# Performance work log

Hardware: AMD Instinct MI355X
Metric: run time of the kernel (lower is better)

Reference implementation:

```python
import jax, jax.numpy as jnp
import numpy as np

N_NODES = 50000
N_EDGES = 600000
CHANNELS = 128
HEADS = 8


def setup_inputs() -> dict:
    key = jax.random.key(0)
    k1, k2, k3 = jax.random.split(key, 3)
    x = jax.random.normal(k1, (N_NODES, CHANNELS), dtype=jnp.float32)
    edge_index = jax.random.randint(k2, (2, N_EDGES), 0, N_NODES, dtype=jnp.int32)
    att = jax.random.normal(k3, (HEADS, 2 * (CHANNELS // HEADS)), dtype=jnp.float32)
    return {"x": x, "edge_index": edge_index, "att": att}


def reference(x, edge_index, att):
    # x: [N, C], edge_index: [2, E], att: [H, 2*D] with D = C // H
    src, dst = edge_index[0], edge_index[1]
    n = x.shape[0]
    h = att.shape[0]
    d = att.shape[1] // 2

    x_src = x[src].reshape(-1, h, d)   # [E, H, D]
    x_dst = x[dst].reshape(-1, h, d)   # [E, H, D]

    # (cat([x_src, x_dst]) * att).sum(-1) == x_src @ att[:, :D] + x_dst @ att[:, D:]
    a_src, a_dst = att[:, :d], att[:, d:]
    alpha = jnp.einsum('ehd,hd->eh', x_src, a_src) + jnp.einsum('ehd,hd->eh', x_dst, a_dst)
    alpha = jnp.where(alpha >= 0, alpha, 0.2 * alpha)  # LeakyReLU(0.2)

    # segment softmax over dst; torch scatter_reduce amax includes the zero init,
    # so the per-node max is max(segment_max, 0)
    seg_max = jax.ops.segment_max(alpha, dst, num_segments=n)  # [N, H]
    seg_max = jnp.maximum(seg_max, 0.0)
    alpha = jnp.exp(alpha - seg_max[dst])
    seg_sum = jax.ops.segment_sum(alpha, dst, num_segments=n)  # [N, H]
    alpha = alpha / jnp.maximum(seg_sum[dst], 1e-10)

    # weighted scatter-add of source features
    weighted = x_src * alpha[..., None]                        # [E, H, D]
    out = jax.ops.segment_sum(weighted, dst, num_segments=n)   # [N, H, D]
    return out.reshape(n, -1)
```

## Files before the change

### kernel.cpp

```cpp
#include <hip/hip_runtime.h>

#define N_NODES  50000
#define N_EDGES  600000
#define CHANNELS 128
#define HEADS    8
#define HEAD_DIM 16
#define CAP      64

#define NBINS    256
#define CHUNK_E  1024
#define NCHUNK   ((N_EDGES + CHUNK_E - 1) / CHUNK_E)
#define SEGCAP   2816
#define NPB      200
#define BPAD     16

#define LOGIT_VB ((N_NODES * (CHANNELS / 8)) / 256)
#define WPB      4

__device__ __forceinline__ unsigned bf16rne(float f) {
    unsigned u = __float_as_uint(f);
    return (u + 0x7FFFu + ((u >> 16) & 1u)) >> 16;
}

__global__ void logit_kernel(const float* __restrict__ x,
                             const float* __restrict__ att,
                             float*          __restrict__ ls8,
                             float*          __restrict__ ld8,
                             unsigned short* __restrict__ xb,
                             int*            __restrict__ bincnt_p) {
    if (blockIdx.x == LOGIT_VB) {
        bincnt_p[threadIdx.x * BPAD] = 0;
        return;
    }
    int gid = blockIdx.x * 256 + threadIdx.x;
    int n  = gid >> 4;
    int c8 = gid & 15;
    int h  = c8 >> 1;
    int j8 = c8 & 1;

    const float4* xp = (const float4*)x + (size_t)gid * 2;
    float4 v0 = xp[0], v1 = xp[1];

    uint4 pk;
    pk.x = bf16rne(v0.x) | (bf16rne(v0.y) << 16);
    pk.y = bf16rne(v0.z) | (bf16rne(v0.w) << 16);
    pk.z = bf16rne(v1.x) | (bf16rne(v1.y) << 16);
    pk.w = bf16rne(v1.z) | (bf16rne(v1.w) << 16);
    ((uint4*)xb)[gid] = pk;

    const float4* att4 = (const float4*)att;
    float4 as0 = att4[h * 8 + j8 * 2],     as1 = att4[h * 8 + j8 * 2 + 1];
    float4 ad0 = att4[h * 8 + 4 + j8 * 2], ad1 = att4[h * 8 + 5 + j8 * 2];
    float ts = v0.x*as0.x + v0.y*as0.y + v0.z*as0.z + v0.w*as0.w
             + v1.x*as1.x + v1.y*as1.y + v1.z*as1.z + v1.w*as1.w;
    float td = v0.x*ad0.x + v0.y*ad0.y + v0.z*ad0.z + v0.w*ad0.w
             + v1.x*ad1.x + v1.y*ad1.y + v1.z*ad1.z + v1.w*ad1.w;
    ts += __shfl_xor(ts, 1, 2);
    td += __shfl_xor(td, 1, 2);
    if (j8 == 0) {
        ls8[n * HEADS + h] = ts;
        ld8[n * HEADS + h] = td;
    }
}

__global__ void binscatter_kernel(const int* __restrict__ src,
                                  const int* __restrict__ dst,
                                  int*       __restrict__ bincnt_p,
                                  unsigned*  __restrict__ ebuf) {
    __shared__ int lh[NBINS];
    __shared__ int lbase[NBINS];
    int b = blockIdx.x;
    int t = threadIdx.x;
    lh[t] = 0;
    __syncthreads();
    int base = b * CHUNK_E;
    unsigned rec[4], bn[4];
#pragma unroll
    for (int k = 0; k < 4; ++k) {
        int e = base + t + k * 256;
        if (e < N_EDGES) {
            int d = dst[e];
            int s = src[e];
            unsigned bin = (unsigned)(d * NBINS) / N_NODES;
            bn[k]  = bin;
            rec[k] = (unsigned)s | ((unsigned)d << 16);
            atomicAdd(&lh[bin], 1);
        } else bn[k] = 0xFFFFFFFFu;
    }
    __syncthreads();
    int cnt_bin = lh[t];
    __syncthreads();
    lbase[t] = (cnt_bin > 0) ? atomicAdd(&bincnt_p[t * BPAD], cnt_bin) : 0;
    lh[t] = 0;
    __syncthreads();
#pragma unroll
    for (int k = 0; k < 4; ++k) {
        if (bn[k] != 0xFFFFFFFFu) {
            int r = atomicAdd(&lh[bn[k]], 1) + lbase[bn[k]];
            if (r < SEGCAP)
                ebuf[(size_t)bn[k] * SEGCAP + r] = rec[k];
        }
    }
}

__global__ void bucket_kernel(const unsigned* __restrict__ ebuf,
                              const int*      __restrict__ bincnt_p,
                              int*            __restrict__ cursor,
                              unsigned short* __restrict__ bucket) {
    __shared__ unsigned short rows[NPB * CAP];
    __shared__ int lcnt[NPB];
    int b = blockIdx.x;
    int t = threadIdx.x;
    int n0 = (b * N_NODES + NBINS - 1) / NBINS;
    int n1 = ((b + 1) * N_NODES + NBINS - 1) / NBINS;
    int nn = n1 - n0;
    if (t < NPB) lcnt[t] = 0;
    __syncthreads();
    int cnt = min(bincnt_p[b * BPAD], SEGCAP);
    for (int i = t; i < cnt; i += 256) {
        unsigned rec = ebuf[(size_t)b * SEGCAP + i];
        int s = (int)(rec & 0xFFFFu);
        int d = (int)(rec >> 16);
        int pos = atomicAdd(&lcnt[d - n0], 1);
        if (pos < CAP) rows[(d - n0) * CAP + pos] = (unsigned short)s;
    }
    __syncthreads();
    int nq = nn * (CAP * 2 / 16);
    uint4* gdst = (uint4*)(bucket + (size_t)n0 * CAP);
    const uint4* lsrc = (const uint4*)rows;
    for (int i = t; i < nq; i += 256) gdst[i] = lsrc[i];
    if (t < nn) cursor[n0 + t] = lcnt[t];
}

__global__ void fused_gat_kernel(const unsigned short* __restrict__ xb,
                                 const float* __restrict__ ls8,
                                 const float* __restrict__ ld8,
                                 const int*   __restrict__ cursor,
                                 const unsigned short* __restrict__ bucket,
                                 float*       __restrict__ out) {
    __shared__ float s_p[WPB * CAP * HEADS];

    int wave = threadIdx.x >> 6;
    int lane = threadIdx.x & 63;
    int n = blockIdx.x * WPB + wave;
    if (n >= N_NODES) return;
    int h = lane >> 3;
    int j = lane & 7;
    int r   = lane >> 4;
    int l16 = lane & 15;
    int h2  = l16 >> 1;

    int   cnt_raw = cursor[n];
    int   myidx   = (int)bucket[(size_t)n * CAP + lane];
    float ldst    = ld8[n * HEADS + h];
    int cnt = (cnt_raw > CAP) ? CAP : cnt_raw;

    float* sp = s_p + wave * (CAP * HEADS);

    float av[8];
    float mymax = -1e30f;
#pragma unroll
    for (int k = 0; k < 8; ++k) {
        int i = j + 8 * k;
        av[k] = -1e30f;
        if (i < cnt) {
            int   s  = __shfl(myidx, i);
            float lg = ls8[s * HEADS + h] + ldst;
            float a  = (lg >= 0.0f) ? lg : 0.2f * lg;
            av[k] = a;
            mymax = fmaxf(mymax, a);
        }
    }
#pragma unroll
    for (int o = 4; o >= 1; o >>= 1) mymax = fmaxf(mymax, __shfl_xor(mymax, o, 8));
    float m = fmaxf(mymax, 0.0f);

    float myl = 0.0f;
#pragma unroll
    for (int k = 0; k < 8; ++k) {
        int i = j + 8 * k;
        if (i < cnt) {
            float p = __expf(av[k] - m);
            sp[i * HEADS + h] = p;
            myl += p;
        }
    }
#pragma unroll
    for (int o = 4; o >= 1; o >>= 1) myl += __shfl_xor(myl, o, 8);

#define LO16(u) __uint_as_float((u) << 16)
#define HI16(u) __uint_as_float((u) & 0xFFFF0000u)
#define LP(kq) ( ((const uint4*)(xb + (size_t)__shfl(myidx, ((4*(kq)+r) < cnt) ? (4*(kq)+r) : 0) * CHANNELS))[l16] )
    uint4 q[4];
#pragma unroll
    for (int k = 0; k < 4; ++k) q[k] = LP(k);

    float a0 = 0.f, a1 = 0.f, a2 = 0.f, a3 = 0.f;
    float a4 = 0.f, a5 = 0.f, a6 = 0.f, a7 = 0.f;
    int nquad = (cnt + 3) >> 2;
    int k = 0;
    for (; k + 2 <= nquad; k += 2) {
#pragma unroll
        for (int u = 0; u < 2; ++u) {
            int e4 = 4 * (k + u) + r;
            float p = (e4 < cnt) ? sp[e4 * HEADS + h2] : 0.0f;
            uint4 qq = q[u];
            a0 += p * LO16(qq.x);
            a1 += p * HI16(qq.x);
            a2 += p * LO16(qq.y);
            a3 += p * HI16(qq.y);
            a4 += p * LO16(qq.z);
            a5 += p * HI16(qq.z);
            a6 += p * LO16(qq.w);
            a7 += p * HI16(qq.w);
        }
        q[0] = q[2]; q[1] = q[3];
        q[2] = LP(k + 4);
        q[3] = LP(k + 5);
    }
    for (; k < nquad; ++k) {
        int e4 = 4 * k + r;
        float p = (e4 < cnt) ? sp[e4 * HEADS + h2] : 0.0f;
        uint4 qq = q[0];
        a0 += p * LO16(qq.x);
        a1 += p * HI16(qq.x);
        a2 += p * LO16(qq.y);
        a3 += p * HI16(qq.y);
        a4 += p * LO16(qq.z);
        a5 += p * HI16(qq.z);
        a6 += p * LO16(qq.w);
        a7 += p * HI16(qq.w);
        q[0] = q[1]; q[1] = q[2]; q[2] = q[3];
    }
#undef LP
#undef LO16
#undef HI16

    a0 += __shfl_xor(a0, 16); a0 += __shfl_xor(a0, 32);
    a1 += __shfl_xor(a1, 16); a1 += __shfl_xor(a1, 32);
    a2 += __shfl_xor(a2, 16); a2 += __shfl_xor(a2, 32);
    a3 += __shfl_xor(a3, 16); a3 += __shfl_xor(a3, 32);
    a4 += __shfl_xor(a4, 16); a4 += __shfl_xor(a4, 32);
    a5 += __shfl_xor(a5, 16); a5 += __shfl_xor(a5, 32);
    a6 += __shfl_xor(a6, 16); a6 += __shfl_xor(a6, 32);
    a7 += __shfl_xor(a7, 16); a7 += __shfl_xor(a7, 32);

    float denom = __shfl(myl, h2 * 8);
    float inv = 1.0f / fmaxf(denom, 1e-10f);

    if (lane < 16) {
        float4 o0 = make_float4(a0 * inv, a1 * inv, a2 * inv, a3 * inv);
        float4 o1 = make_float4(a4 * inv, a5 * inv, a6 * inv, a7 * inv);
        float4* op = (float4*)(out + (size_t)n * CHANNELS) + l16 * 2;
        op[0] = o0;
        op[1] = o1;
    }
}

extern "C" void kernel_launch(void* const* d_in, const int* in_sizes, int n_in,
                              void* d_out, int out_size, void* d_ws, size_t ws_size,
                              hipStream_t stream) {
    const float* x   = (const float*)d_in[0];
    const int*   ei  = (const int*)  d_in[1];
    const float* att = (const float*)d_in[2];
    const int* src = ei;
    const int* dst = ei + N_EDGES;
    float* out = (float*)d_out;

    int*            bincnt_p = (int*)d_ws;
    unsigned*       ebuf     = (unsigned*)(bincnt_p + (size_t)NBINS * BPAD);
    int*            cursor   = (int*)(ebuf + (size_t)NBINS * SEGCAP);
    unsigned short* bucket   = (unsigned short*)(cursor + N_NODES);
    float*          ls8      = (float*)(bucket + (size_t)N_NODES * CAP);
    float*          ld8      = ls8 + (size_t)N_NODES * HEADS;
    unsigned short* xb       = (unsigned short*)(ld8 + (size_t)N_NODES * HEADS);

    logit_kernel<<<LOGIT_VB + 1, 256, 0, stream>>>(x, att, ls8, ld8, xb, bincnt_p);
    binscatter_kernel<<<NCHUNK, 256, 0, stream>>>(src, dst, bincnt_p, ebuf);
    bucket_kernel<<<NBINS, 256, 0, stream>>>(ebuf, bincnt_p, cursor, bucket);
    fused_gat_kernel<<<(N_NODES + WPB - 1) / WPB, 64 * WPB, 0, stream>>>(
        xb, ls8, ld8, cursor, bucket, out);
}
```

Baseline: 143.0 us.

## Fuse binning with logit prep and bucketing with aggregation into two kernels

The pipeline drops from four kernels to two. Edge binning now runs in the same launch as the logit/bf16 conversion, writing into fixed per-(bin,chunk) slots with per-chunk counts, which removes the global atomics and the zeroing step. The bucket build is fused into the aggregation kernel, so each block builds its node rows in shared memory and consumes them directly instead of writing and re-reading a global bucket array. In exchange, only 1024 blocks of 4 waves do the aggregation, each looping over about 49 nodes, which may lower parallelism and load balance. Per-chunk slot caps (24) could also silently drop edges when a chunk is skewed.

Result: faster. 136.4 us (-4.6%).

```diff
diff --git a/kernel.cpp b/kernel.cpp
--- a/kernel.cpp
+++ b/kernel.cpp
@@ -7,32 +7,59 @@
 #define HEAD_DIM 16
 #define CAP      64
 
-#define NBINS    256
-#define CHUNK_E  1024
+#define NBINS    1024
+#define CHUNK_E  4096
 #define NCHUNK   ((N_EDGES + CHUNK_E - 1) / CHUNK_E)
-#define SEGCAP   2816
-#define NPB      200
-#define BPAD     16
+#define CAPC     24
+#define NPB      52
 
 #define LOGIT_VB ((N_NODES * (CHANNELS / 8)) / 256)
-#define WPB      4
+#define NW       4
 
 __device__ __forceinline__ unsigned bf16rne(float f) {
     unsigned u = __float_as_uint(f);
     return (u + 0x7FFFu + ((u >> 16) & 1u)) >> 16;
 }
 
-__global__ void logit_kernel(const float* __restrict__ x,
-                             const float* __restrict__ att,
-                             float*          __restrict__ ls8,
-                             float*          __restrict__ ld8,
-                             unsigned short* __restrict__ xb,
-                             int*            __restrict__ bincnt_p) {
-    if (blockIdx.x == LOGIT_VB) {
-        bincnt_p[threadIdx.x * BPAD] = 0;
+__global__ void prep_kernel(const float* __restrict__ x,
+                            const float* __restrict__ att,
+                            const int*   __restrict__ src,
+                            const int*   __restrict__ dst,
+                            float*          __restrict__ ls8,
+                            float*          __restrict__ ld8,
+                            unsigned short* __restrict__ xb,
+                            unsigned*       __restrict__ ebuf,
+                            int*            __restrict__ cc) {
+    int b = blockIdx.x;
+    int t = threadIdx.x;
+    if (b < NCHUNK) {
+        __shared__ int lh[NBINS];
+#pragma unroll
+        for (int k = 0; k < NBINS / 256; ++k) lh[t + k * 256] = 0;
+        __syncthreads();
+        int base = b * CHUNK_E;
+#pragma unroll 4
+        for (int k = 0; k < CHUNK_E / 256; ++k) {
+            int e = base + t + k * 256;
+            if (e < N_EDGES) {
+                int d = dst[e];
+                int s = src[e];
+                unsigned bin = ((unsigned)d * NBINS) / N_NODES;
+                int r = atomicAdd(&lh[bin], 1);
+                if (r < CAPC)
+                    ebuf[((size_t)bin * NCHUNK + b) * CAPC + r] =
+                        (unsigned)s | ((unsigned)d << 16);
+            }
+        }
+        __syncthreads();
+#pragma unroll
+        for (int k = 0; k < NBINS / 256; ++k) {
+            int bin = t + k * 256;
+            cc[(size_t)bin * NCHUNK + b] = min(lh[bin], CAPC);
+        }
         return;
     }
-    int gid = blockIdx.x * 256 + threadIdx.x;
+    int gid = (b - NCHUNK) * 256 + t;
     int n  = gid >> 4;
     int c8 = gid & 15;
     int h  = c8 >> 1;
@@ -63,148 +90,121 @@
     }
 }
 
-__global__ void binscatter_kernel(const int* __restrict__ src,
-                                  const int* __restrict__ dst,
-                                  int*       __restrict__ bincnt_p,
-                                  unsigned*  __restrict__ ebuf) {
-    __shared__ int lh[NBINS];
-    __shared__ int lbase[NBINS];
-    int b = blockIdx.x;
-    int t = threadIdx.x;
-    lh[t] = 0;
-    __syncthreads();
-    int base = b * CHUNK_E;
-    unsigned rec[4], bn[4];
-#pragma unroll
-    for (int k = 0; k < 4; ++k) {
-        int e = base + t + k * 256;
-        if (e < N_EDGES) {
-            int d = dst[e];
-            int s = src[e];
-            unsigned bin = (unsigned)(d * NBINS) / N_NODES;
-            bn[k]  = bin;
-            rec[k] = (unsigned)s | ((unsigned)d << 16);
-            atomicAdd(&lh[bin], 1);
-        } else bn[k] = 0xFFFFFFFFu;
-    }
-    __syncthreads();
-    int cnt_bin = lh[t];
-    __syncthreads();
-    lbase[t] = (cnt_bin > 0) ? atomicAdd(&bincnt_p[t * BPAD], cnt_bin) : 0;
-    lh[t] = 0;
-    __syncthreads();
-#pragma unroll
-    for (int k = 0; k < 4; ++k) {
-        if (bn[k] != 0xFFFFFFFFu) {
-            int r = atomicAdd(&lh[bn[k]], 1) + lbase[bn[k]];
-            if (r < SEGCAP)
-                ebuf[(size_t)bn[k] * SEGCAP + r] = rec[k];
-        }
-    }
-}
-
-__global__ void bucket_kernel(const unsigned* __restrict__ ebuf,
-                              const int*      __restrict__ bincnt_p,
-                              int*            __restrict__ cursor,
-                              unsigned short* __restrict__ bucket) {
+__global__ void aggregate_kernel(const unsigned* __restrict__ ebuf,
+                                 const int*      __restrict__ cc,
+                                 const unsigned short* __restrict__ xb,
+                                 const float* __restrict__ ls8,
+                                 const float* __restrict__ ld8,
+                                 float*       __restrict__ out) {
     __shared__ unsigned short rows[NPB * CAP];
-    __shared__ int lcnt[NPB];
+    __shared__ int   lcnt[NPB];
+    __shared__ int   lcc[NCHUNK];
+    __shared__ float s_p[NW * CAP * HEADS];
+
     int b = blockIdx.x;
     int t = threadIdx.x;
     int n0 = (b * N_NODES + NBINS - 1) / NBINS;
     int n1 = ((b + 1) * N_NODES + NBINS - 1) / NBINS;
     int nn = n1 - n0;
     if (t < NPB) lcnt[t] = 0;
+    if (t < NCHUNK) lcc[t] = cc[(size_t)b * NCHUNK + t];
     __syncthreads();
-    int cnt = min(bincnt_p[b * BPAD], SEGCAP);
-    for (int i = t; i < cnt; i += 256) {
-        unsigned rec = ebuf[(size_t)b * SEGCAP + i];
-        int s = (int)(rec & 0xFFFFu);
-        int d = (int)(rec >> 16);
-        int pos = atomicAdd(&lcnt[d - n0], 1);
-        if (pos < CAP) rows[(d - n0) * CAP + pos] = (unsigned short)s;
+
+    const unsigned* seg = ebuf + (size_t)b * NCHUNK * CAPC;
+    for (int p = t; p < NCHUNK * CAPC; p += 256) {
+        int c    = p / CAPC;
+        int slot = p - c * CAPC;
+        if (slot < lcc[c]) {
+            unsigned rec = seg[p];
+            int s = (int)(rec & 0xFFFFu);
+            int d = (int)(rec >> 16);
+            int pos = atomicAdd(&lcnt[d - n0], 1);
+            if (pos < CAP) rows[(d - n0) * CAP + pos] = (unsigned short)s;
+        }
     }
     __syncthreads();
-    int nq = nn * (CAP * 2 / 16);
-    uint4* gdst = (uint4*)(bucket + (size_t)n0 * CAP);
-    const uint4* lsrc = (const uint4*)rows;
-    for (int i = t; i < nq; i += 256) gdst[i] = lsrc[i];
-    if (t < nn) cursor[n0 + t] = lcnt[t];
-}
-
-__global__ void fused_gat_kernel(const unsigned short* __restrict__ xb,
-                                 const float* __restrict__ ls8,
-                                 const float* __restrict__ ld8,
-                                 const int*   __restrict__ cursor,
-                                 const unsigned short* __restrict__ bucket,
-                                 float*       __restrict__ out) {
-    __shared__ float s_p[WPB * CAP * HEADS];
-
-    int wave = threadIdx.x >> 6;
-    int lane = threadIdx.x & 63;
-    int n = blockIdx.x * WPB + wave;
-    if (n >= N_NODES) return;
+
+    int wave = t >> 6;
+    int lane = t & 63;
     int h = lane >> 3;
     int j = lane & 7;
     int r   = lane >> 4;
     int l16 = lane & 15;
     int h2  = l16 >> 1;
-
-    int   cnt_raw = cursor[n];
-    int   myidx   = (int)bucket[(size_t)n * CAP + lane];
-    float ldst    = ld8[n * HEADS + h];
-    int cnt = (cnt_raw > CAP) ? CAP : cnt_raw;
-
     float* sp = s_p + wave * (CAP * HEADS);
 
-    float av[8];
-    float mymax = -1e30f;
-#pragma unroll
-    for (int k = 0; k < 8; ++k) {
-        int i = j + 8 * k;
-        av[k] = -1e30f;
-        if (i < cnt) {
-            int   s  = __shfl(myidx, i);
-            float lg = ls8[s * HEADS + h] + ldst;
-            float a  = (lg >= 0.0f) ? lg : 0.2f * lg;
-            av[k] = a;
-            mymax = fmaxf(mymax, a);
-        }
-    }
-#pragma unroll
-    for (int o = 4; o >= 1; o >>= 1) mymax = fmaxf(mymax, __shfl_xor(mymax, o, 8));
-    float m = fmaxf(mymax, 0.0f);
-
-    float myl = 0.0f;
-#pragma unroll
-    for (int k = 0; k < 8; ++k) {
-        int i = j + 8 * k;
-        if (i < cnt) {
-            float p = __expf(av[k] - m);
-            sp[i * HEADS + h] = p;
-            myl += p;
-        }
-    }
-#pragma unroll
-    for (int o = 4; o >= 1; o >>= 1) myl += __shfl_xor(myl, o, 8);
+    for (int idx = wave; idx < nn; idx += NW) {
+        int n = n0 + idx;
+        int cnt_raw = lcnt[idx];
+        int cnt = (cnt_raw > CAP) ? CAP : cnt_raw;
+        int myidx = (int)rows[idx * CAP + lane];
+        float ldst = ld8[n * HEADS + h];
+
+        float av[8];
+        float mymax = -1e30f;
+#pragma unroll
+        for (int k = 0; k < 8; ++k) {
+            int i = j + 8 * k;
+            av[k] = -1e30f;
+            if (i < cnt) {
+                int   s  = __shfl(myidx, i);
+                float lg = ls8[s * HEADS + h] + ldst;
+                float a  = (lg >= 0.0f) ? lg : 0.2f * lg;
+                av[k] = a;
+                mymax = fmaxf(mymax, a);
+            }
+        }
+#pragma unroll
+        for (int o = 4; o >= 1; o >>= 1) mymax = fmaxf(mymax, __shfl_xor(mymax, o, 8));
+        float m = fmaxf(mymax, 0.0f);
+
+        float myl = 0.0f;
+#pragma unroll
+        for (int k = 0; k < 8; ++k) {
+            int i = j + 8 * k;
+            if (i < cnt) {
+                float p = __expf(av[k] - m);
+                sp[i * HEADS + h] = p;
+                myl += p;
+            }
+        }
+#pragma unroll
+        for (int o = 4; o >= 1; o >>= 1) myl += __shfl_xor(myl, o, 8);
 
 #define LO16(u) __uint_as_float((u) << 16)
 #define HI16(u) __uint_as_float((u) & 0xFFFF0000u)
 #define LP(kq) ( ((const uint4*)(xb + (size_t)__shfl(myidx, ((4*(kq)+r) < cnt) ? (4*(kq)+r) : 0) * CHANNELS))[l16] )
-    uint4 q[4];
-#pragma unroll
-    for (int k = 0; k < 4; ++k) q[k] = LP(k);
-
-    float a0 = 0.f, a1 = 0.f, a2 = 0.f, a3 = 0.f;
-    float a4 = 0.f, a5 = 0.f, a6 = 0.f, a7 = 0.f;
-    int nquad = (cnt + 3) >> 2;
-    int k = 0;
-    for (; k + 2 <= nquad; k += 2) {
-#pragma unroll
-        for (int u = 0; u < 2; ++u) {
-            int e4 = 4 * (k + u) + r;
+        uint4 q[4];
+#pragma unroll
+        for (int k = 0; k < 4; ++k) q[k] = LP(k);
+
+        float a0 = 0.f, a1 = 0.f, a2 = 0.f, a3 = 0.f;
+        float a4 = 0.f, a5 = 0.f, a6 = 0.f, a7 = 0.f;
+        int nquad = (cnt + 3) >> 2;
+        int k = 0;
+        for (; k + 2 <= nquad; k += 2) {
+#pragma unroll
+            for (int u = 0; u < 2; ++u) {
+                int e4 = 4 * (k + u) + r;
+                float p = (e4 < cnt) ? sp[e4 * HEADS + h2] : 0.0f;
+                uint4 qq = q[u];
+                a0 += p * LO16(qq.x);
+                a1 += p * HI16(qq.x);
+                a2 += p * LO16(qq.y);
+                a3 += p * HI16(qq.y);
+                a4 += p * LO16(qq.z);
+                a5 += p * HI16(qq.z);
+                a6 += p * LO16(qq.w);
+                a7 += p * HI16(qq.w);
+            }
+            q[0] = q[2]; q[1] = q[3];
+            q[2] = LP(k + 4);
+            q[3] = LP(k + 5);
+        }
+        for (; k < nquad; ++k) {
+            int e4 = 4 * k + r;
             float p = (e4 < cnt) ? sp[e4 * HEADS + h2] : 0.0f;
-            uint4 qq = q[u];
+            uint4 qq = q[0];
             a0 += p * LO16(qq.x);
             a1 += p * HI16(qq.x);
             a2 += p * LO16(qq.y);
@@ -213,47 +213,31 @@
             a5 += p * HI16(qq.z);
             a6 += p * LO16(qq.w);
             a7 += p * HI16(qq.w);
-        }
-        q[0] = q[2]; q[1] = q[3];
-        q[2] = LP(k + 4);
-        q[3] = LP(k + 5);
-    }
-    for (; k < nquad; ++k) {
-        int e4 = 4 * k + r;
-        float p = (e4 < cnt) ? sp[e4 * HEADS + h2] : 0.0f;
-        uint4 qq = q[0];
-        a0 += p * LO16(qq.x);
-        a1 += p * HI16(qq.x);
-        a2 += p * LO16(qq.y);
-        a3 += p * HI16(qq.y);
-        a4 += p * LO16(qq.z);
-        a5 += p * HI16(qq.z);
-        a6 += p * LO16(qq.w);
-        a7 += p * HI16(qq.w);
-        q[0] = q[1]; q[1] = q[2]; q[2] = q[3];
-    }
+            q[0] = q[1]; q[1] = q[2]; q[2] = q[3];
+        }
 #undef LP
 #undef LO16
 #undef HI16
 
-    a0 += __shfl_xor(a0, 16); a0 += __shfl_xor(a0, 32);
-    a1 += __shfl_xor(a1, 16); a1 += __shfl_xor(a1, 32);
-    a2 += __shfl_xor(a2, 16); a2 += __shfl_xor(a2, 32);
-    a3 += __shfl_xor(a3, 16); a3 += __shfl_xor(a3, 32);
-    a4 += __shfl_xor(a4, 16); a4 += __shfl_xor(a4, 32);
-    a5 += __shfl_xor(a5, 16); a5 += __shfl_xor(a5, 32);
-    a6 += __shfl_xor(a6, 16); a6 += __shfl_xor(a6, 32);
-    a7 += __shfl_xor(a7, 16); a7 += __shfl_xor(a7, 32);
-
-    float denom = __shfl(myl, h2 * 8);
-    float inv = 1.0f / fmaxf(denom, 1e-10f);
-
-    if (lane < 16) {
-        float4 o0 = make_float4(a0 * inv, a1 * inv, a2 * inv, a3 * inv);
-        float4 o1 = make_float4(a4 * inv, a5 * inv, a6 * inv, a7 * inv);
-        float4* op = (float4*)(out + (size_t)n * CHANNELS) + l16 * 2;
-        op[0] = o0;
-        op[1] = o1;
+        a0 += __shfl_xor(a0, 16); a0 += __shfl_xor(a0, 32);
+        a1 += __shfl_xor(a1, 16); a1 += __shfl_xor(a1, 32);
+        a2 += __shfl_xor(a2, 16); a2 += __shfl_xor(a2, 32);
+        a3 += __shfl_xor(a3, 16); a3 += __shfl_xor(a3, 32);
+        a4 += __shfl_xor(a4, 16); a4 += __shfl_xor(a4, 32);
+        a5 += __shfl_xor(a5, 16); a5 += __shfl_xor(a5, 32);
+        a6 += __shfl_xor(a6, 16); a6 += __shfl_xor(a6, 32);
+        a7 += __shfl_xor(a7, 16); a7 += __shfl_xor(a7, 32);
+
+        float denom = __shfl(myl, h2 * 8);
+        float inv = 1.0f / fmaxf(denom, 1e-10f);
+
+        if (lane < 16) {
+            float4 o0 = make_float4(a0 * inv, a1 * inv, a2 * inv, a3 * inv);
+            float4 o1 = make_float4(a4 * inv, a5 * inv, a6 * inv, a7 * inv);
+            float4* op = (float4*)(out + (size_t)n * CHANNELS) + l16 * 2;
+            op[0] = o0;
+            op[1] = o1;
+        }
     }
 }
 
@@ -267,17 +251,13 @@
     const int* dst = ei + N_EDGES;
     float* out = (float*)d_out;
 
-    int*            bincnt_p = (int*)d_ws;
-    unsigned*       ebuf     = (unsigned*)(bincnt_p + (size_t)NBINS * BPAD);
-    int*            cursor   = (int*)(ebuf + (size_t)NBINS * SEGCAP);
-    unsigned short* bucket   = (unsigned short*)(cursor + N_NODES);
-    float*          ls8      = (float*)(bucket + (size_t)N_NODES * CAP);
-    float*          ld8      = ls8 + (size_t)N_NODES * HEADS;
-    unsigned short* xb       = (unsigned short*)(ld8 + (size_t)N_NODES * HEADS);
-
-    logit_kernel<<<LOGIT_VB + 1, 256, 0, stream>>>(x, att, ls8, ld8, xb, bincnt_p);
-    binscatter_kernel<<<NCHUNK, 256, 0, stream>>>(src, dst, bincnt_p, ebuf);
-    bucket_kernel<<<NBINS, 256, 0, stream>>>(ebuf, bincnt_p, cursor, bucket);
-    fused_gat_kernel<<<(N_NODES + WPB - 1) / WPB, 64 * WPB, 0, stream>>>(
-        xb, ls8, ld8, cursor, bucket, out);
-}
+    unsigned*       ebuf = (unsigned*)d_ws;
+    int*            cc   = (int*)(ebuf + (size_t)NBINS * NCHUNK * CAPC);
+    float*          ls8  = (float*)(cc + (size_t)NBINS * NCHUNK);
+    float*          ld8  = ls8 + (size_t)N_NODES * HEADS;
+    unsigned short* xb   = (unsigned short*)(ld8 + (size_t)N_NODES * HEADS);
+
+    prep_kernel<<<NCHUNK + LOGIT_VB, 256, 0, stream>>>(
+        x, att, src, dst, ls8, ld8, xb, ebuf, cc);
+    aggregate_kernel<<<NBINS, 256, 0, stream>>>(ebuf, cc, xb, ls8, ld8, out);
+}
```
